# Kernel tuning notes

Measured on AMD Instinct MI355X. Metric: run time of the kernel, lower is better.

Reference implementation:

```python
import jax, jax.numpy as jnp
import numpy as np

T = 5
NORM_GROUPS = 4
EPS = 1e-5


def setup_inputs() -> dict:
    key = jax.random.key(0)
    inputs = jax.random.normal(key, (16384, 2048), dtype=jnp.float32)
    return {"inputs": inputs}


def reference(inputs):
    k = inputs.shape
    C = k[-1]
    g = NORM_GROUPS
    d = C // g
    # (g, N, d) where N = total_elems / C * ... = fan_in for a 2D weight
    Z = inputs.reshape(g, -1, d)
    Zc = Z - jnp.mean(Z, axis=1, keepdims=True)           # center over samples
    S = jnp.einsum('gnd,gne->gde', Zc, Zc)                # (g, d, d) covariance
    eye = jnp.eye(d, dtype=inputs.dtype)[None]            # (1, d, d)
    S = S + EPS * eye
    norm_S = jnp.sqrt(jnp.sum(S * S, axis=(1, 2), keepdims=True))  # Frobenius
    S = S / norm_S
    # Newton-Schulz iterations: B_{t+1} = 1.5 B_t - 0.5 B_t^3 S
    B = jnp.broadcast_to(eye, S.shape)
    for _ in range(T):
        B3 = (B @ B) @ B
        B = 1.5 * B - 0.5 * (B3 @ S)
    # W = B Zc^T / sqrt(||S||_F)  -> (g, d, N)
    W = (B @ jnp.swapaxes(Zc, 1, 2)) / jnp.sqrt(norm_S)
    return jnp.swapaxes(W, 1, 2).reshape(k)
```

## Files before the change

### kernel.cpp

```cpp
#include <hip/hip_runtime.h>
#include <hip/hip_bf16.h>

#define NG 4
#define DD 512
#define NN 16384
#define EPSV 1e-5f
#define GRP_ELEMS ((size_t)NN * DD)
#define MAT_ELEMS ((size_t)DD * DD)
#define KCHUNKS 8

typedef __attribute__((ext_vector_type(8))) short bf16x8;
typedef __attribute__((ext_vector_type(4))) float f32x4;

__device__ __forceinline__ ushort f2b(float f) {
    union { float f; unsigned u; } x; x.f = f;
    unsigned r = (x.u + 0x7fffu + ((x.u >> 16) & 1u)) >> 16;
    return (ushort)r;
}
__device__ __forceinline__ float b2f(ushort u) {
    union { unsigned u; float f; } x; x.u = ((unsigned)u) << 16;
    return x.f;
}
__device__ __forceinline__ void load_lds16(const ushort* g, ushort* l) {
    __builtin_amdgcn_global_load_lds(
        (const __attribute__((address_space(1))) void*)g,
        (__attribute__((address_space(3))) void*)l, 16, 0, 0);
}

__global__ __launch_bounds__(256) void colsum_kernel(const float* __restrict__ Z,
                                                     float* __restrict__ cs) {
    int c = blockIdx.x * 256 + threadIdx.x;
    int a = c >> 9;
    int d = c & 511;
    const float* p = Z + (size_t)a * GRP_ELEMS + (size_t)blockIdx.y * 512 * DD + d;
    float s = 0.f;
    #pragma unroll 8
    for (int n = 0; n < 512; ++n) s += p[(size_t)n * DD];
    atomicAdd(&cs[c], s);
}

__global__ __launch_bounds__(256) void convT_kernel(const float* __restrict__ Z,
                                                    const float* __restrict__ cs,
                                                    ushort* __restrict__ ZbT) {
    __shared__ float tile[64][65];
    int g = blockIdx.z;
    int n0 = blockIdx.x * 64;
    int d0 = blockIdx.y * 64;
    int t = threadIdx.x;
    int c4 = (t & 15) * 4;
    int r = t >> 4;
    float m0 = cs[g * DD + d0 + c4 + 0] * (1.f / (float)NN);
    float m1 = cs[g * DD + d0 + c4 + 1] * (1.f / (float)NN);
    float m2 = cs[g * DD + d0 + c4 + 2] * (1.f / (float)NN);
    float m3 = cs[g * DD + d0 + c4 + 3] * (1.f / (float)NN);
    const float* Zg = Z + (size_t)g * GRP_ELEMS;
    #pragma unroll
    for (int p = 0; p < 4; ++p) {
        int rr = r + p * 16;
        float4 v = *(const float4*)&Zg[(size_t)(n0 + rr) * DD + d0 + c4];
        tile[rr][c4 + 0] = v.x - m0;
        tile[rr][c4 + 1] = v.y - m1;
        tile[rr][c4 + 2] = v.z - m2;
        tile[rr][c4 + 3] = v.w - m3;
    }
    __syncthreads();
    ushort* Og = ZbT + (size_t)g * GRP_ELEMS;
    #pragma unroll
    for (int p = 0; p < 4; ++p) {
        int dl = r + p * 16;
        int nl = c4;
        ushort4 o;
        o.x = f2b(tile[nl + 0][dl]);
        o.y = f2b(tile[nl + 1][dl]);
        o.z = f2b(tile[nl + 2][dl]);
        o.w = f2b(tile[nl + 3][dl]);
        *(ushort4*)&Og[(size_t)(d0 + dl) * NN + n0 + nl] = o;
    }
}

__global__ __launch_bounds__(256) void convN_kernel(const float* __restrict__ Z,
                                                    const float* __restrict__ cs,
                                                    ushort* __restrict__ Zb) {
    size_t i4 = (size_t)blockIdx.x * 256 + threadIdx.x;
    size_t base = i4 * 4;
    int g = (int)(base >> 23);
    int d = (int)(base & 511);
    float4 v = *(const float4*)&Z[base];
    const float* c = cs + g * DD + d;
    ushort4 o;
    o.x = f2b(v.x - c[0] * (1.f / (float)NN));
    o.y = f2b(v.y - c[1] * (1.f / (float)NN));
    o.z = f2b(v.z - c[2] * (1.f / (float)NN));
    o.w = f2b(v.w - c[3] * (1.f / (float)NN));
    *(ushort4*)&Zb[base] = o;
}

template<int MODE>
__global__ __launch_bounds__(256) void gemm_bt(
    const ushort* __restrict__ Ap, const ushort* __restrict__ Bp,
    float* __restrict__ outF, ushort* __restrict__ outU,
    const ushort* __restrict__ Curp, const float* __restrict__ nrm,
    int Mtiles, int lda, int ldb, int K, size_t grpA, size_t grpB)
{
    __shared__ __align__(16) ushort As[128 * 32];
    __shared__ __align__(16) ushort Bs[128 * 32];
    const int g = blockIdx.z;
    const int tm = (blockIdx.x % Mtiles) * 128;
    const int tn = (blockIdx.x / Mtiles) * 128;
    const int kstart = blockIdx.y * K;
    const ushort* Ag = Ap + (size_t)g * grpA;
    const ushort* Bg = Bp + (size_t)g * grpB;
    const int t = threadIdx.x;
    const int wave = t >> 6, lane = t & 63;
    const int lr = lane >> 2;
    const int lc = (lane & 3) * 8;
    const int s0 = wave * 2;
    const int qm = (wave & 1) * 64, qn = (wave >> 1) * 64;
    const int fm = lane & 15;
    const int fk = (lane >> 4) * 8;

    const ushort* a0p = Ag + (size_t)(tm + s0 * 16 + lr) * lda + lc;
    const ushort* a1p = Ag + (size_t)(tm + s0 * 16 + 16 + lr) * lda + lc;
    const ushort* b0p = Bg + (size_t)(tn + s0 * 16 + lr) * ldb + lc;
    const ushort* b1p = Bg + (size_t)(tn + s0 * 16 + 16 + lr) * ldb + lc;
    ushort* lA0 = As + s0 * 512;
    ushort* lA1 = As + s0 * 512 + 512;
    ushort* lB0 = Bs + s0 * 512;
    ushort* lB1 = Bs + s0 * 512 + 512;

    f32x4 acc[4][4] = {};
    for (int k0 = kstart; k0 < kstart + K; k0 += 32) {
        load_lds16(a0p + k0, lA0);
        load_lds16(a1p + k0, lA1);
        load_lds16(b0p + k0, lB0);
        load_lds16(b1p + k0, lB1);
        __syncthreads();
        bf16x8 af[4], bfr[4];
        #pragma unroll
        for (int i = 0; i < 4; ++i) {
            af[i]  = *(const bf16x8*)&As[(qm + i * 16 + fm) * 32 + fk];
            bfr[i] = *(const bf16x8*)&Bs[(qn + i * 16 + fm) * 32 + fk];
        }
        #pragma unroll
        for (int i = 0; i < 4; ++i)
            #pragma unroll
            for (int j = 0; j < 4; ++j)
                acc[i][j] = __builtin_amdgcn_mfma_f32_16x16x32_bf16(
                    af[i], bfr[j], acc[i][j], 0, 0, 0);
        __syncthreads();
    }

    const int cn0 = tn + qn + fm;
    const int cm0 = tm + qm + (lane >> 4) * 4;
    if (MODE == 0) {
        float* O = outF + (size_t)(blockIdx.y * NG + g) * MAT_ELEMS;
        #pragma unroll
        for (int i = 0; i < 4; ++i)
            #pragma unroll
            for (int r = 0; r < 4; ++r) {
                size_t row = (size_t)(cm0 + i * 16 + r) * DD;
                #pragma unroll
                for (int j = 0; j < 4; ++j)
                    O[row + cn0 + j * 16] = acc[i][j][r];
            }
    } else if (MODE == 1) {
        ushort* O = outU + (size_t)g * MAT_ELEMS;
        #pragma unroll
        for (int i = 0; i < 4; ++i)
            #pragma unroll
            for (int r = 0; r < 4; ++r) {
                size_t row = (size_t)(cm0 + i * 16 + r) * DD;
                #pragma unroll
                for (int j = 0; j < 4; ++j)
                    O[row + cn0 + j * 16] = f2b(acc[i][j][r]);
            }
    } else if (MODE == 2) {
        const ushort* C = Curp + (size_t)g * MAT_ELEMS;
        ushort* O = outU + (size_t)g * MAT_ELEMS;
        float sc = 0.5f * rsqrtf(nrm[g]);
        #pragma unroll
        for (int i = 0; i < 4; ++i)
            #pragma unroll
            for (int r = 0; r < 4; ++r) {
                size_t row = (size_t)(cm0 + i * 16 + r) * DD;
                #pragma unroll
                for (int j = 0; j < 4; ++j) {
                    size_t off = row + cn0 + j * 16;
                    O[off] = f2b(1.5f * b2f(C[off]) - sc * acc[i][j][r]);
                }
            }
    } else {
        float* O = outF + (size_t)g * GRP_ELEMS;
        float sc = rsqrtf(sqrtf(nrm[g]));
        #pragma unroll
        for (int i = 0; i < 4; ++i)
            #pragma unroll
            for (int r = 0; r < 4; ++r) {
                size_t row = (size_t)(cm0 + i * 16 + r) * DD;
                #pragma unroll
                for (int j = 0; j < 4; ++j)
                    O[row + cn0 + j * 16] = sc * acc[i][j][r];
            }
    }
}

__global__ __launch_bounds__(256) void reduce_fin(const float* __restrict__ Sp,
                                                  ushort* __restrict__ Sb,
                                                  float* __restrict__ nrmP) {
    __shared__ float wsum[4];
    int g = blockIdx.z;
    int idx = blockIdx.x * 256 + threadIdx.x;
    float v = 0.f;
    #pragma unroll
    for (int c = 0; c < KCHUNKS; ++c)
        v += Sp[(size_t)(c * NG + g) * MAT_ELEMS + idx];
    int i = idx >> 9, j = idx & 511;
    if (i == j) v += EPSV;
    Sb[(size_t)g * MAT_ELEMS + idx] = f2b(v);
    float ss = v * v;
    #pragma unroll
    for (int o = 32; o; o >>= 1) ss += __shfl_down(ss, o, 64);
    if ((threadIdx.x & 63) == 0) wsum[threadIdx.x >> 6] = ss;
    __syncthreads();
    if (threadIdx.x == 0)
        nrmP[(size_t)g * 1024 + blockIdx.x] = wsum[0] + wsum[1] + wsum[2] + wsum[3];
}

__global__ __launch_bounds__(256) void nrm_fin(const float* __restrict__ nrmP,
                                               float* __restrict__ nrm) {
    __shared__ float wsum[4];
    int g = blockIdx.x;
    float s = 0.f;
    #pragma unroll
    for (int p = 0; p < 4; ++p)
        s += nrmP[(size_t)g * 1024 + p * 256 + threadIdx.x];
    #pragma unroll
    for (int o = 32; o; o >>= 1) s += __shfl_down(s, o, 64);
    if ((threadIdx.x & 63) == 0) wsum[threadIdx.x >> 6] = s;
    __syncthreads();
    if (threadIdx.x == 0) nrm[g] = wsum[0] + wsum[1] + wsum[2] + wsum[3];
}

__global__ __launch_bounds__(256) void initB_kernel(const ushort* __restrict__ Sb,
                                                    const float* __restrict__ nrm,
                                                    ushort* __restrict__ B0) {
    int g = blockIdx.z;
    int idx = blockIdx.x * 256 + threadIdx.x;
    int i = idx >> 9, j = idx & 511;
    float invnu = rsqrtf(nrm[g]);
    size_t off = (size_t)g * MAT_ELEMS + idx;
    float v = ((i == j) ? 1.5f : 0.f) - 0.5f * invnu * b2f(Sb[off]);
    B0[off] = f2b(v);
}

extern "C" void kernel_launch(void* const* d_in, const int* in_sizes, int n_in,
                              void* d_out, int out_size, void* d_ws, size_t ws_size,
                              hipStream_t stream) {
    const float* Z = (const float*)d_in[0];
    float* out = (float*)d_out;
    float* ws = (float*)d_ws;

    float* cs   = ws;
    float* nrm  = ws + 2048;
    float* nrmP = ws + 2112;
    ushort* Zbuf = (ushort*)(ws + 8192);
    float* Spart = ws + 8192 + (NG * GRP_ELEMS / 2);
    ushort* Sb = (ushort*)(Spart + (size_t)KCHUNKS * NG * MAT_ELEMS);
    ushort* B0 = Sb + NG * MAT_ELEMS;
    ushort* B1 = B0 + NG * MAT_ELEMS;
    ushort* Pb = B1 + NG * MAT_ELEMS;
    ushort* Qb = Pb + NG * MAT_ELEMS;

    hipMemsetAsync(ws, 0, 2048 * sizeof(float), stream);

    colsum_kernel<<<dim3(8, 32), 256, 0, stream>>>(Z, cs);
    convT_kernel<<<dim3(256, 8, NG), 256, 0, stream>>>(Z, cs, Zbuf);

    gemm_bt<0><<<dim3(16, KCHUNKS, NG), 256, 0, stream>>>(
        Zbuf, Zbuf, Spart, nullptr, nullptr, nullptr,
        4, NN, NN, NN / KCHUNKS, GRP_ELEMS, GRP_ELEMS);

    reduce_fin<<<dim3(1024, 1, NG), 256, 0, stream>>>(Spart, Sb, nrmP);
    nrm_fin<<<dim3(NG), 256, 0, stream>>>(nrmP, nrm);

    convN_kernel<<<dim3(32768), 256, 0, stream>>>(Z, cs, Zbuf);

    initB_kernel<<<dim3(1024, 1, NG), 256, 0, stream>>>(Sb, nrm, B0);

    ushort* cur = B0; ushort* nxt = B1;
    for (int it = 0; it < 4; ++it) {
        gemm_bt<1><<<dim3(16, 1, NG), 256, 0, stream>>>(
            cur, cur, nullptr, Pb, nullptr, nullptr, 4, DD, DD, DD, MAT_ELEMS, MAT_ELEMS);
        gemm_bt<1><<<dim3(16, 1, NG), 256, 0, stream>>>(
            Pb, cur, nullptr, Qb, nullptr, nullptr, 4, DD, DD, DD, MAT_ELEMS, MAT_ELEMS);
        gemm_bt<2><<<dim3(16, 1, NG), 256, 0, stream>>>(
            Qb, Sb, nullptr, nxt, cur, nrm, 4, DD, DD, DD, MAT_ELEMS, MAT_ELEMS);
        ushort* tmp = cur; cur = nxt; nxt = tmp;
    }

    gemm_bt<3><<<dim3(512, 1, NG), 256, 0, stream>>>(
        Zbuf, cur, out, nullptr, nullptr, nrm, 128, DD, DD, DD, GRP_ELEMS, MAT_ELEMS);
}
```

Before: 581.1 us.

## Fold mean-centering into covariance and output GEMM epilogues, fuse conversions

Removes the separate column-sum pass and the second conversion kernel. A single transpose kernel now reads Z once and writes both transposed and row-major bf16 copies of the uncentered data, plus per-block column partial sums. Centering is applied algebraically instead: N·mu·muᵀ is subtracted from the covariance in the reduction, and B·mu is subtracted in the final GEMM epilogue. This cuts extra passes over the 128 MB input, but applying bf16 rounding to uncentered data and subtracting afterward risks cancellation error.

```diff
diff --git a/kernel.cpp b/kernel.cpp
--- a/kernel.cpp
+++ b/kernel.cpp
@@ -27,21 +27,10 @@
         (__attribute__((address_space(3))) void*)l, 16, 0, 0);
 }
 
-__global__ __launch_bounds__(256) void colsum_kernel(const float* __restrict__ Z,
-                                                     float* __restrict__ cs) {
-    int c = blockIdx.x * 256 + threadIdx.x;
-    int a = c >> 9;
-    int d = c & 511;
-    const float* p = Z + (size_t)a * GRP_ELEMS + (size_t)blockIdx.y * 512 * DD + d;
-    float s = 0.f;
-    #pragma unroll 8
-    for (int n = 0; n < 512; ++n) s += p[(size_t)n * DD];
-    atomicAdd(&cs[c], s);
-}
-
 __global__ __launch_bounds__(256) void convT_kernel(const float* __restrict__ Z,
-                                                    const float* __restrict__ cs,
-                                                    ushort* __restrict__ ZbT) {
+                                                    ushort* __restrict__ ZbT,
+                                                    ushort* __restrict__ Zb,
+                                                    float* __restrict__ csP) {
     __shared__ float tile[64][65];
     int g = blockIdx.z;
     int n0 = blockIdx.x * 64;
@@ -49,19 +38,19 @@
     int t = threadIdx.x;
     int c4 = (t & 15) * 4;
     int r = t >> 4;
-    float m0 = cs[g * DD + d0 + c4 + 0] * (1.f / (float)NN);
-    float m1 = cs[g * DD + d0 + c4 + 1] * (1.f / (float)NN);
-    float m2 = cs[g * DD + d0 + c4 + 2] * (1.f / (float)NN);
-    float m3 = cs[g * DD + d0 + c4 + 3] * (1.f / (float)NN);
     const float* Zg = Z + (size_t)g * GRP_ELEMS;
+    ushort* ZbG = Zb + (size_t)g * GRP_ELEMS;
     #pragma unroll
     for (int p = 0; p < 4; ++p) {
         int rr = r + p * 16;
         float4 v = *(const float4*)&Zg[(size_t)(n0 + rr) * DD + d0 + c4];
-        tile[rr][c4 + 0] = v.x - m0;
-        tile[rr][c4 + 1] = v.y - m1;
-        tile[rr][c4 + 2] = v.z - m2;
-        tile[rr][c4 + 3] = v.w - m3;
+        tile[rr][c4 + 0] = v.x;
+        tile[rr][c4 + 1] = v.y;
+        tile[rr][c4 + 2] = v.z;
+        tile[rr][c4 + 3] = v.w;
+        ushort4 o;
+        o.x = f2b(v.x); o.y = f2b(v.y); o.z = f2b(v.z); o.w = f2b(v.w);
+        *(ushort4*)&ZbG[(size_t)(n0 + rr) * DD + d0 + c4] = o;
     }
     __syncthreads();
     ushort* Og = ZbT + (size_t)g * GRP_ELEMS;
@@ -76,23 +65,23 @@
         o.w = f2b(tile[nl + 3][dl]);
         *(ushort4*)&Og[(size_t)(d0 + dl) * NN + n0 + nl] = o;
     }
-}
-
-__global__ __launch_bounds__(256) void convN_kernel(const float* __restrict__ Z,
-                                                    const float* __restrict__ cs,
-                                                    ushort* __restrict__ Zb) {
-    size_t i4 = (size_t)blockIdx.x * 256 + threadIdx.x;
-    size_t base = i4 * 4;
-    int g = (int)(base >> 23);
-    int d = (int)(base & 511);
-    float4 v = *(const float4*)&Z[base];
-    const float* c = cs + g * DD + d;
-    ushort4 o;
-    o.x = f2b(v.x - c[0] * (1.f / (float)NN));
-    o.y = f2b(v.y - c[1] * (1.f / (float)NN));
-    o.z = f2b(v.z - c[2] * (1.f / (float)NN));
-    o.w = f2b(v.w - c[3] * (1.f / (float)NN));
-    *(ushort4*)&Zb[base] = o;
+    if (t < 64) {
+        float s = 0.f;
+        #pragma unroll 8
+        for (int n = 0; n < 64; ++n) s += tile[n][t];
+        csP[((size_t)g * 256 + blockIdx.x) * 512 + d0 + t] = s;
+    }
+}
+
+__global__ __launch_bounds__(256) void colsum_fin(const float* __restrict__ csP,
+                                                  float* __restrict__ cs) {
+    int c = blockIdx.x * 256 + threadIdx.x;
+    int g = c >> 9, d = c & 511;
+    const float* p = csP + (size_t)g * 256 * 512 + d;
+    float s = 0.f;
+    #pragma unroll 8
+    for (int b = 0; b < 256; ++b) s += p[(size_t)b * 512];
+    cs[c] = s * (1.f / (float)NN);
 }
 
 template<int MODE>
@@ -100,6 +89,7 @@
     const ushort* __restrict__ Ap, const ushort* __restrict__ Bp,
     float* __restrict__ outF, ushort* __restrict__ outU,
     const ushort* __restrict__ Curp, const float* __restrict__ nrm,
+    const float* __restrict__ bmup,
     int Mtiles, int lda, int ldb, int K, size_t grpA, size_t grpB)
 {
     __shared__ __align__(16) ushort As[128 * 32];
@@ -192,6 +182,10 @@
     } else {
         float* O = outF + (size_t)g * GRP_ELEMS;
         float sc = rsqrtf(sqrtf(nrm[g]));
+        const float* bm = bmup + g * DD;
+        float bmj[4];
+        #pragma unroll
+        for (int j = 0; j < 4; ++j) bmj[j] = bm[cn0 + j * 16];
         #pragma unroll
         for (int i = 0; i < 4; ++i)
             #pragma unroll
@@ -199,12 +193,13 @@
                 size_t row = (size_t)(cm0 + i * 16 + r) * DD;
                 #pragma unroll
                 for (int j = 0; j < 4; ++j)
-                    O[row + cn0 + j * 16] = sc * acc[i][j][r];
+                    O[row + cn0 + j * 16] = sc * (acc[i][j][r] - bmj[j]);
             }
     }
 }
 
 __global__ __launch_bounds__(256) void reduce_fin(const float* __restrict__ Sp,
+                                                  const float* __restrict__ cs,
                                                   ushort* __restrict__ Sb,
                                                   float* __restrict__ nrmP) {
     __shared__ float wsum[4];
@@ -215,6 +210,7 @@
     for (int c = 0; c < KCHUNKS; ++c)
         v += Sp[(size_t)(c * NG + g) * MAT_ELEMS + idx];
     int i = idx >> 9, j = idx & 511;
+    v -= (float)NN * cs[g * DD + i] * cs[g * DD + j];
     if (i == j) v += EPSV;
     Sb[(size_t)g * MAT_ELEMS + idx] = f2b(v);
     float ss = v * v;
@@ -253,6 +249,25 @@
     B0[off] = f2b(v);
 }
 
+__global__ __launch_bounds__(256) void bmu_kernel(const ushort* __restrict__ B,
+                                                  const float* __restrict__ cs,
+                                                  float* __restrict__ bmu) {
+    int g = blockIdx.z;
+    int wave = threadIdx.x >> 6, lane = threadIdx.x & 63;
+    int i = blockIdx.x * 4 + wave;
+    const ushort* Bg = B + (size_t)g * MAT_ELEMS + (size_t)i * DD + lane * 8;
+    const float* mu = cs + g * DD + lane * 8;
+    ushort4 u0 = *(const ushort4*)(Bg);
+    ushort4 u1 = *(const ushort4*)(Bg + 4);
+    float s = b2f(u0.x) * mu[0] + b2f(u0.y) * mu[1]
+            + b2f(u0.z) * mu[2] + b2f(u0.w) * mu[3]
+            + b2f(u1.x) * mu[4] + b2f(u1.y) * mu[5]
+            + b2f(u1.z) * mu[6] + b2f(u1.w) * mu[7];
+    #pragma unroll
+    for (int o = 32; o; o >>= 1) s += __shfl_down(s, o, 64);
+    if (lane == 0) bmu[g * DD + i] = s;
+}
+
 extern "C" void kernel_launch(void* const* d_in, const int* in_sizes, int n_in,
                               void* d_out, int out_size, void* d_ws, size_t ws_size,
                               hipStream_t stream) {
@@ -262,42 +277,47 @@
 
     float* cs   = ws;
     float* nrm  = ws + 2048;
-    float* nrmP = ws + 2112;
-    ushort* Zbuf = (ushort*)(ws + 8192);
-    float* Spart = ws + 8192 + (NG * GRP_ELEMS / 2);
+    float* bmu  = ws + 2112;
+    float* nrmP = ws + 4160;
+    float* csP  = ws + 8256;
+    ushort* ZbT = (ushort*)(ws + 532544);
+    ushort* Zb  = (ushort*)(ws + 17309760);
+    float* Spart = ws + 34086976;
     ushort* Sb = (ushort*)(Spart + (size_t)KCHUNKS * NG * MAT_ELEMS);
     ushort* B0 = Sb + NG * MAT_ELEMS;
     ushort* B1 = B0 + NG * MAT_ELEMS;
     ushort* Pb = B1 + NG * MAT_ELEMS;
     ushort* Qb = Pb + NG * MAT_ELEMS;
 
-    hipMemsetAsync(ws, 0, 2048 * sizeof(float), stream);
-
-    colsum_kernel<<<dim3(8, 32), 256, 0, stream>>>(Z, cs);
-    convT_kernel<<<dim3(256, 8, NG), 256, 0, stream>>>(Z, cs, Zbuf);
+    convT_kernel<<<dim3(256, 8, NG), 256, 0, stream>>>(Z, ZbT, Zb, csP);
+    colsum_fin<<<dim3(8), 256, 0, stream>>>(csP, cs);
 
     gemm_bt<0><<<dim3(16, KCHUNKS, NG), 256, 0, stream>>>(
-        Zbuf, Zbuf, Spart, nullptr, nullptr, nullptr,
+        ZbT, ZbT, Spart, nullptr, nullptr, nullptr, nullptr,
         4, NN, NN, NN / KCHUNKS, GRP_ELEMS, GRP_ELEMS);
 
-    reduce_fin<<<dim3(1024, 1, NG), 256, 0, stream>>>(Spart, Sb, nrmP);
+    reduce_fin<<<dim3(1024, 1, NG), 256, 0, stream>>>(Spart, cs, Sb, nrmP);
     nrm_fin<<<dim3(NG), 256, 0, stream>>>(nrmP, nrm);
-
-    convN_kernel<<<dim3(32768), 256, 0, stream>>>(Z, cs, Zbuf);
 
     initB_kernel<<<dim3(1024, 1, NG), 256, 0, stream>>>(Sb, nrm, B0);
 
     ushort* cur = B0; ushort* nxt = B1;
     for (int it = 0; it < 4; ++it) {
         gemm_bt<1><<<dim3(16, 1, NG), 256, 0, stream>>>(
-            cur, cur, nullptr, Pb, nullptr, nullptr, 4, DD, DD, DD, MAT_ELEMS, MAT_ELEMS);
+            cur, cur, nullptr, Pb, nullptr, nullptr, nullptr,
+            4, DD, DD, DD, MAT_ELEMS, MAT_ELEMS);
         gemm_bt<1><<<dim3(16, 1, NG), 256, 0, stream>>>(
-            Pb, cur, nullptr, Qb, nullptr, nullptr, 4, DD, DD, DD, MAT_ELEMS, MAT_ELEMS);
+            Pb, cur, nullptr, Qb, nullptr, nullptr, nullptr,
+            4, DD, DD, DD, MAT_ELEMS, MAT_ELEMS);
         gemm_bt<2><<<dim3(16, 1, NG), 256, 0, stream>>>(
-            Qb, Sb, nullptr, nxt, cur, nrm, 4, DD, DD, DD, MAT_ELEMS, MAT_ELEMS);
+            Qb, Sb, nullptr, nxt, cur, nrm, nullptr,
+            4, DD, DD, DD, MAT_ELEMS, MAT_ELEMS);
         ushort* tmp = cur; cur = nxt; nxt = tmp;
     }
 
+    bmu_kernel<<<dim3(128, 1, NG), 256, 0, stream>>>(cur, cs, bmu);
+
     gemm_bt<3><<<dim3(512, 1, NG), 256, 0, stream>>>(
-        Zbuf, cur, out, nullptr, nullptr, nrm, 128, DD, DD, DD, GRP_ELEMS, MAT_ELEMS);
-}
+        Zb, cur, out, nullptr, nullptr, nrm, bmu,
+        128, DD, DD, DD, GRP_ELEMS, MAT_ELEMS);
+}
```

Measured after the change: 553.1 us. -4.8%, faster.
